# Kernel tuning notes

Measured on AMD Instinct MI355X. Metric: run time of the kernel, lower is better.

The kernel has to match this reference:

```python
import jax, jax.numpy as jnp
import numpy as np


def setup_inputs() -> dict:
    key = jax.random.key(0)
    ks = jax.random.split(key, 6)
    B, C, W, H = 8, 512, 64, 64
    return {
        "x": jax.random.normal(ks[0], (B, C, W, H), dtype=jnp.float32),
        "proj_query": jax.random.normal(ks[1], (C, W, H), dtype=jnp.float32),
        "key_w": jax.random.normal(ks[2], (C, C), dtype=jnp.float32) * 0.02,
        "key_b": jax.random.normal(ks[3], (C,), dtype=jnp.float32) * 0.02,
        "value_w": jax.random.normal(ks[4], (C, C), dtype=jnp.float32) * 0.02,
        "value_b": jax.random.normal(ks[5], (C,), dtype=jnp.float32) * 0.02,
        "gamma": jnp.ones((1,), dtype=jnp.float32),
    }


def reference(x, proj_query, key_w, key_b, value_w, value_b, gamma):
    B, C, W, H = x.shape
    N = W * H
    # fixed memory query: (C, N); torch builds B x N x C via permute
    q = proj_query.reshape(C, N)
    # 1x1 convs == per-pixel channel matmuls
    k = jnp.einsum('oc,bchw->bohw', key_w, x) + key_b[None, :, None, None]
    v = jnp.einsum('oc,bchw->bohw', value_w, x) + value_b[None, :, None, None]
    k = k.reshape(B, C, N)
    v = v.reshape(B, C, N)
    # energy = bmm(key [B,C,N], query^T [N,C]) -> B x C x C (channel attention)
    energy = jnp.einsum('bcn,dn->bcd', k, q)
    attention = jax.nn.softmax(energy, axis=-1)
    # out = bmm(attention^T [B,C,C], value [B,C,N]) -> B x C x N
    out = jnp.einsum('bdc,bdn->bcn', attention, v)
    out = out.reshape(B, C, W, H)
    return gamma * out + x
```

## Files before the change

### kernel.cpp

```cpp
#include <hip/hip_runtime.h>

typedef unsigned short u16;
typedef unsigned int u32;
typedef unsigned long long u64;
typedef _Float16 f16x8 __attribute__((ext_vector_type(8)));
typedef float f32x4 __attribute__((ext_vector_type(4)));

__device__ __forceinline__ u16 f2h(float f) {
  union { _Float16 h; u16 u; } c; c.h = (_Float16)f; return c.u;
}
__device__ __forceinline__ float h2f(u16 v) {
  union { u16 u; _Float16 h; } c; c.u = v; return (float)c.h;
}

__device__ __forceinline__ f32x4 mfma16(f16x8 a, f16x8 b, f32x4 c) {
  return __builtin_amdgcn_mfma_f32_16x16x32_f16(a, b, c, 0, 0, 0);
}

__device__ __forceinline__ void ld8f(const float* s, u16* o) {
  float4 a = *(const float4*)s;
  float4 b = *(const float4*)(s + 4);
  o[0] = f2h(a.x); o[1] = f2h(a.y); o[2] = f2h(a.z); o[3] = f2h(a.w);
  o[4] = f2h(b.x); o[5] = f2h(b.y); o[6] = f2h(b.z); o[7] = f2h(b.w);
}

__device__ __forceinline__ void cvt8(float4 a, float4 b, u16* o) {
  o[0] = f2h(a.x); o[1] = f2h(a.y); o[2] = f2h(a.z); o[3] = f2h(a.w);
  o[4] = f2h(b.x); o[5] = f2h(b.y); o[6] = f2h(b.z); o[7] = f2h(b.w);
}

__device__ __forceinline__ void glds16(const u16* g, u16* l) {
  __builtin_amdgcn_global_load_lds(
      reinterpret_cast<const __attribute__((address_space(1))) u32*>(reinterpret_cast<u64>(g)),
      reinterpret_cast<__attribute__((address_space(3))) u32*>(reinterpret_cast<u64>(l)),
      16, 0, 0);
}

template<int TM, int TN, int WM, int WN, int DEPTH>
__device__ __forceinline__ void gemm_core(const u16* __restrict__ A, int lda,
                                          const u16* __restrict__ B, int ldb,
                                          int ksteps, u16* sA, u16* sB, f32x4 acc[TM][TN]) {
  constexpr int NT = WM * WN * 64;
  constexpr int BM = WM * TM * 16, BN = WN * TN * 16;
  constexpr int TILEA = BM * 32, TILEB = BN * 32;
  constexpr int APF = (BM * 4) / NT, BPF = (BN * 4) / NT;
  constexpr int VPI = APF + BPF;
  constexpr int PF = DEPTH - 2;
  static_assert(PF == 1 || PF == 2, "");
  static_assert(APF >= 1 && BPF >= 1, "");

  const int t = threadIdx.x;
  const int lane = t & 63, wave = t >> 6;
  const int wm = wave / WN, wn = wave % WN;
  const int m16 = lane & 15, q4 = lane >> 4;

  int aoff[APF], asl[APF];
#pragma unroll
  for (int p = 0; p < APF; ++p) {
    int s = p * NT + t, row = s >> 2;
    int kc = (s & 3) ^ ((row >> 1) & 3);
    aoff[p] = row * lda + kc * 8;
    asl[p] = (p * NT + (wave << 6)) * 8;
  }
  int boff[BPF], bsl[BPF];
#pragma unroll
  for (int p = 0; p < BPF; ++p) {
    int s = p * NT + t, row = s >> 2;
    int kc = (s & 3) ^ ((row >> 1) & 3);
    boff[p] = row * ldb + kc * 8;
    bsl[p] = (p * NT + (wave << 6)) * 8;
  }

  int aro[TM], bro[TN];
#pragma unroll
  for (int i = 0; i < TM; ++i) {
    int row = wm * TM * 16 + i * 16 + m16;
    aro[i] = row * 32 + ((q4 ^ ((row >> 1) & 3)) << 3);
  }
#pragma unroll
  for (int j = 0; j < TN; ++j) {
    int row = wn * TN * 16 + j * 16 + m16;
    bro[j] = row * 32 + ((q4 ^ ((row >> 1) & 3)) << 3);
  }

#pragma unroll
  for (int j = 0; j < PF; ++j) {
    const u16* Aj = A + j * 32;
    u16* aS = sA + j * TILEA;
#pragma unroll
    for (int p = 0; p < APF; ++p) glds16(Aj + aoff[p], aS + asl[p]);
    const u16* Bj = B + j * 32;
    u16* bS = sB + j * TILEB;
#pragma unroll
    for (int p = 0; p < BPF; ++p) glds16(Bj + boff[p], bS + bsl[p]);
  }

  int cur = 0, stg = PF;
#pragma unroll 1
  for (int kt = 0; kt < ksteps; ++kt) {
    if (kt + PF < ksteps) {
      const u16* An = A + (size_t)(kt + PF) * 32;
      u16* aS = sA + stg * TILEA;
#pragma unroll
      for (int p = 0; p < APF; ++p) glds16(An + aoff[p], aS + asl[p]);
      const u16* Bn = B + (size_t)(kt + PF) * 32;
      u16* bS = sB + stg * TILEB;
#pragma unroll
      for (int p = 0; p < BPF; ++p) glds16(Bn + boff[p], bS + bsl[p]);
    }
    if (PF == 2 && kt + 2 < ksteps)
      asm volatile("s_waitcnt vmcnt(%0)" :: "n"(2 * VPI) : "memory");
    else if (kt + 1 < ksteps)
      asm volatile("s_waitcnt vmcnt(%0)" :: "n"(VPI) : "memory");
    else
      asm volatile("s_waitcnt vmcnt(0)" ::: "memory");
    __builtin_amdgcn_s_barrier();
    __builtin_amdgcn_sched_barrier(0);

    const u16* aR = sA + cur * TILEA;
    const u16* bR = sB + cur * TILEB;
    f16x8 af[TM], bv[TN];
#pragma unroll
    for (int i = 0; i < TM; ++i) af[i] = *(const f16x8*)&aR[aro[i]];
#pragma unroll
    for (int j = 0; j < TN; ++j) bv[j] = *(const f16x8*)&bR[bro[j]];
#pragma unroll
    for (int i = 0; i < TM; ++i)
#pragma unroll
      for (int j = 0; j < TN; ++j)
        acc[i][j] = mfma16(af[i], bv[j], acc[i][j]);

    cur = (cur + 1 == DEPTH) ? 0 : cur + 1;
    stg = (stg + 1 == DEPTH) ? 0 : stg + 1;
  }
}

__global__ __launch_bounds__(256) void prep_all_kernel(const float* __restrict__ x,
                                                       u16* __restrict__ xh, u16* __restrict__ xhT,
                                                       const float* __restrict__ q, u16* __restrict__ qh,
                                                       float* __restrict__ qs,
                                                       const float* __restrict__ vw, u16* __restrict__ vwT,
                                                       const float* __restrict__ kw, u16* __restrict__ kwh,
                                                       float* __restrict__ beta) {
  __shared__ __align__(16) u16 T[2 * 64 * 72];
  int blk = blockIdx.x, t = threadIdx.x;
  if (blk < 512) {
    int nt = blk & 63, b = blk >> 6;
    int s = t & 31;
    int c = (t >> 5) * 8;
    const float* xbase = x + ((size_t)b * 512 + 2 * s) * 4096 + nt * 64 + c;
    int rr = t >> 2, og = t & 3;

    float4 ca0 = *(const float4*)xbase;
    float4 ca1 = *(const float4*)(xbase + 4);
    float4 cb0 = *(const float4*)(xbase + 4096);
    float4 cb1 = *(const float4*)(xbase + 4100);

#pragma unroll 1
    for (int ot = 0; ot < 8; ++ot) {
      float4 na0, na1, nb0, nb1;
      if (ot < 7) {
        const float* np = xbase + (size_t)(ot + 1) * 64 * 4096;
        na0 = *(const float4*)np;
        na1 = *(const float4*)(np + 4);
        nb0 = *(const float4*)(np + 4096);
        nb1 = *(const float4*)(np + 4100);
      }
      u16 r0[8], r1[8];
      cvt8(ca0, ca1, r0);
      cvt8(cb0, cb1, r1);

      u16* xq = xh + ((size_t)b * 512 + ot * 64 + 2 * s) * 4096 + nt * 64 + c;
      *(int4*)xq = *(int4*)r0;
      *(int4*)(xq + 4096) = *(int4*)r1;

      u32* Tw = (u32*)(T + (ot & 1) * 4608);
#pragma unroll
      for (int e = 0; e < 8; ++e)
        Tw[(c + e) * 36 + s] = (u32)r0[e] | ((u32)r1[e] << 16);
      __syncthreads();

      const u16* Tr = T + (ot & 1) * 4608;
      int4 v0 = *(const int4*)&Tr[rr * 72 + og * 16];
      int4 v1 = *(const int4*)&Tr[rr * 72 + og * 16 + 8];
      u16* xo = xhT + ((size_t)b * 4096 + nt * 64 + rr) * 512 + ot * 64 + og * 16;
      *(int4*)xo = v0;
      *(int4*)(xo + 8) = v1;

      ca0 = na0; ca1 = na1; cb0 = nb0; cb1 = nb1;
    }
  } else if (blk < 1024) {
    int row = blk - 512;
    float s = 0.f;
#pragma unroll
    for (int p = 0; p < 2; ++p) {
      size_t i = (size_t)row * 4096 + p * 2048 + t * 8;
      u16 o[8];
      ld8f(q + i, o);
#pragma unroll
      for (int e = 0; e < 8; ++e) s += h2f(o[e]);
      *(int4*)&qh[i] = *(int4*)o;
    }
    for (int off = 32; off; off >>= 1) s += __shfl_xor(s, off);
    __shared__ float wsum[4];
    if ((t & 63) == 0) wsum[t >> 6] = s;
    __syncthreads();
    if (t == 0) qs[row] = wsum[0] + wsum[1] + wsum[2] + wsum[3];
  } else if (blk < 1280) {
    int bi = blk - 1024;
    u16* sT = T;
    int bx = bi & 15, by = bi >> 4;
#pragma unroll
    for (int p = 0; p < 4; ++p) {
      int idx = p * 256 + t; int r = idx >> 5, c = idx & 31;
      sT[r * 33 + c] = f2h(vw[(size_t)(by * 32 + r) * 512 + bx * 32 + c]);
    }
    __syncthreads();
#pragma unroll
    for (int p = 0; p < 4; ++p) {
      int idx = p * 256 + t; int r = idx >> 5, c = idx & 31;
      vwT[(size_t)(bx * 32 + r) * 512 + by * 32 + c] = sT[c * 33 + r];
    }
  } else if (blk < 1408) {
    size_t i = ((size_t)(blk - 1280) * 256 + t) * 8;
    u16 o[8];
    ld8f(kw + i, o);
    *(int4*)&kwh[i] = *(int4*)o;
  } else {
    for (int i = t; i < 4096; i += 256) beta[i] = 0.f;
  }
}

__global__ __launch_bounds__(256) void sgemm_kernel(const u16* __restrict__ qh, const u16* __restrict__ xh,
                                                    float* __restrict__ Sp0, float* __restrict__ Sp1) {
  __shared__ __align__(16) u16 sA[4 * 128 * 32], sB[4 * 128 * 32];
  int rt = blockIdx.x, jt = blockIdx.y, ks = blockIdx.z;
  int b = rt >> 2, o0 = (rt & 3) * 128;
  f32x4 acc[4][4];
#pragma unroll
  for (int i = 0; i < 4; ++i)
#pragma unroll
    for (int j = 0; j < 4; ++j) acc[i][j] = (f32x4){0.f, 0.f, 0.f, 0.f};
  gemm_core<4, 4, 2, 2, 4>(qh + (size_t)jt * 128 * 4096 + (size_t)ks * 2048, 4096,
                           xh + ((size_t)b * 512 + o0) * 4096 + (size_t)ks * 2048, 4096,
                           64, sA, sB, acc);

  const int t = threadIdx.x, lane = t & 63, wave = t >> 6;
  const int wm = wave >> 1, wn = wave & 1, m16 = lane & 15, q4 = lane >> 4;
  float* Sp = ks ? Sp1 : Sp0;
  float* Ob = Sp + (size_t)b * 262144;
#pragma unroll
  for (int i = 0; i < 4; ++i)
#pragma unroll
    for (int j = 0; j < 4; ++j)
#pragma unroll
      for (int r = 0; r < 4; ++r) {
        int y = jt * 128 + wm * 64 + i * 16 + q4 * 4 + r;
        int o = o0 + wn * 64 + j * 16 + m16;
        Ob[(size_t)y * 512 + o] = acc[i][j][r];
      }
}

__global__ __launch_bounds__(256) void sreduce_kernel(const float* __restrict__ Sp0,
                                                      const float* __restrict__ Sp1,
                                                      u16* __restrict__ Sh) {
  size_t i = ((size_t)blockIdx.x * 256 + threadIdx.x) * 8;
  float4 a0 = *(const float4*)(Sp0 + i);
  float4 a1 = *(const float4*)(Sp0 + i + 4);
  float4 b0 = *(const float4*)(Sp1 + i);
  float4 b1 = *(const float4*)(Sp1 + i + 4);
  a0.x += b0.x; a0.y += b0.y; a0.z += b0.z; a0.w += b0.w;
  a1.x += b1.x; a1.y += b1.y; a1.z += b1.z; a1.w += b1.w;
  u16 o[8];
  cvt8(a0, a1, o);
  *(int4*)&Sh[i] = *(int4*)o;
}

__global__ __launch_bounds__(256) void egemm_kernel(const u16* __restrict__ kwh, const u16* __restrict__ Sh,
                                                    float* __restrict__ E) {
  __shared__ __align__(16) u16 sA[4 * 64 * 32], sB[4 * 64 * 32];
  int xt = blockIdx.x >> 3, yt = blockIdx.x & 7, b = blockIdx.y;
  f32x4 acc[2][2];
#pragma unroll
  for (int i = 0; i < 2; ++i)
#pragma unroll
    for (int j = 0; j < 2; ++j) acc[i][j] = (f32x4){0.f, 0.f, 0.f, 0.f};
  gemm_core<2, 2, 2, 2, 4>(kwh + (size_t)xt * 64 * 512, 512,
                           Sh + (size_t)b * 262144 + (size_t)yt * 64 * 512, 512, 16, sA, sB, acc);

  const int t = threadIdx.x, lane = t & 63, wave = t >> 6;
  const int wm = wave >> 1, wn = wave & 1, m16 = lane & 15, q4 = lane >> 4;
  float* O = E + ((size_t)b * 512 + xt * 64) * 512 + yt * 64;
#pragma unroll
  for (int i = 0; i < 2; ++i)
#pragma unroll
    for (int j = 0; j < 2; ++j)
#pragma unroll
      for (int r = 0; r < 4; ++r) {
        int row = wm * 32 + i * 16 + q4 * 4 + r;
        int col = wn * 32 + j * 16 + m16;
        O[(size_t)row * 512 + col] = acc[i][j][r];
      }
}

__global__ __launch_bounds__(256) void softmax_kernel(const float* __restrict__ E, const float* __restrict__ qs,
                                                      const float* __restrict__ kb, const float* __restrict__ vb,
                                                      u16* __restrict__ attT, float* __restrict__ beta) {
  __shared__ float sE[16 * 516];
  __shared__ float sM[16], sS[16];
  int i0 = blockIdx.x * 16, b = blockIdx.y, t = threadIdx.x;
  const float* Eb = E + ((size_t)b * 512 + i0) * 512;
  for (int ch = 0; ch < 32; ++ch) {
    int idx = ch * 256 + t;
    int row = idx >> 9, col = idx & 511;
    sE[row * 516 + col] = Eb[(size_t)row * 512 + col] + kb[i0 + row] * qs[col];
  }
  __syncthreads();
  {
    int row = t >> 4, sub = t & 15;
    float mx = -1e30f;
    for (int ii = 0; ii < 32; ++ii) mx = fmaxf(mx, sE[row * 516 + sub + ii * 16]);
    for (int off = 8; off; off >>= 1) mx = fmaxf(mx, __shfl_xor(mx, off));
    float sm = 0.f;
    for (int ii = 0; ii < 32; ++ii) sm += __expf(sE[row * 516 + sub + ii * 16] - mx);
    for (int off = 8; off; off >>= 1) sm += __shfl_xor(sm, off);
    if (sub == 0) { sM[row] = mx; sS[row] = 1.f / sm; }
  }
  __syncthreads();
  float vbr = vb[i0 + (t & 15)];
  u16* Ob = attT + (size_t)b * 262144;
  for (int ch = 0; ch < 32; ++ch) {
    int idx = ch * 256 + t;
    int r = idx & 15, j = idx >> 4;
    float a = __expf(sE[r * 516 + j] - sM[r]) * sS[r];
    Ob[(size_t)j * 512 + i0 + r] = f2h(a);
    float part = a * vbr;
    for (int off = 8; off; off >>= 1) part += __shfl_xor(part, off);
    if (r == 0) atomicAdd(&beta[b * 512 + j], part);
  }
}

__global__ __launch_bounds__(256) void wgemm_kernel(const u16* __restrict__ attT, const u16* __restrict__ vwT,
                                                    u16* __restrict__ W) {
  __shared__ __align__(16) u16 sA[4 * 64 * 32], sB[4 * 64 * 32];
  int ct = blockIdx.x >> 3, ot = blockIdx.x & 7, b = blockIdx.y;
  f32x4 acc[2][2];
#pragma unroll
  for (int i = 0; i < 2; ++i)
#pragma unroll
    for (int j = 0; j < 2; ++j) acc[i][j] = (f32x4){0.f, 0.f, 0.f, 0.f};
  gemm_core<2, 2, 2, 2, 4>(attT + (size_t)b * 262144 + (size_t)ct * 64 * 512, 512,
                           vwT + (size_t)ot * 64 * 512, 512, 16, sA, sB, acc);

  const int t = threadIdx.x, lane = t & 63, wave = t >> 6;
  const int wm = wave >> 1, wn = wave & 1, m16 = lane & 15, q4 = lane >> 4;
  u16* O = W + (size_t)b * 262144 + (size_t)(ct * 64) * 512 + ot * 64;
#pragma unroll
  for (int i = 0; i < 2; ++i)
#pragma unroll
    for (int j = 0; j < 2; ++j)
#pragma unroll
      for (int r = 0; r < 4; ++r) {
        int row = wm * 32 + i * 16 + q4 * 4 + r;
        int col = wn * 32 + j * 16 + m16;
        O[(size_t)row * 512 + col] = f2h(acc[i][j][r]);
      }
}

__global__ __launch_bounds__(256) void outgemm_kernel(const u16* __restrict__ W, const u16* __restrict__ xhT,
                                                      const float* __restrict__ x, const float* __restrict__ beta,
                                                      const float* __restrict__ gm, float* __restrict__ out) {
  __shared__ __align__(16) u16 sA[4 * 128 * 32], sB[4 * 128 * 32];
  int nt = blockIdx.x, ct = blockIdx.y, b = blockIdx.z;
  f32x4 acc[4][4];
#pragma unroll
  for (int i = 0; i < 4; ++i)
#pragma unroll
    for (int j = 0; j < 4; ++j) acc[i][j] = (f32x4){0.f, 0.f, 0.f, 0.f};
  gemm_core<4, 4, 2, 2, 4>(W + (size_t)b * 262144 + (size_t)ct * 128 * 512, 512,
                           xhT + (size_t)b * 2097152 + (size_t)nt * 128 * 512, 512, 16, sA, sB, acc);

  const int t = threadIdx.x, lane = t & 63, wave = t >> 6;
  const int wm = wave >> 1, wn = wave & 1, m16 = lane & 15, q4 = lane >> 4;
  float g = gm[0];
#pragma unroll
  for (int i = 0; i < 4; ++i)
#pragma unroll
    for (int j = 0; j < 4; ++j)
#pragma unroll
      for (int r = 0; r < 4; ++r) {
        int c = ct * 128 + wm * 64 + i * 16 + q4 * 4 + r;
        int n = nt * 128 + wn * 64 + j * 16 + m16;
        size_t idx = (size_t)b * 2097152 + (size_t)c * 4096 + n;
        out[idx] = g * (acc[i][j][r] + beta[b * 512 + c]) + x[idx];
      }
}

extern "C" void kernel_launch(void* const* d_in, const int* in_sizes, int n_in,
                              void* d_out, int out_size, void* d_ws, size_t ws_size,
                              hipStream_t stream) {
  const float* x  = (const float*)d_in[0];
  const float* pq = (const float*)d_in[1];
  const float* kw = (const float*)d_in[2];
  const float* kb = (const float*)d_in[3];
  const float* vw = (const float*)d_in[4];
  const float* vb = (const float*)d_in[5];
  const float* gm = (const float*)d_in[6];
  float* out = (float*)d_out;

  char* ws = (char*)d_ws;
  u16*   xh   = (u16*)(ws);
  u16*   qh   = (u16*)(ws + (32ull << 20));
  u16*   Sh   = (u16*)(ws + (36ull << 20));
  u16*   W    = (u16*)(ws + (36ull << 20));
  float* E    = (float*)(ws + (40ull << 20));
  float* Sp0  = (float*)(ws + (40ull << 20));
  u16*   attT = (u16*)(ws + (48ull << 20));
  u16*   kwh  = (u16*)(ws + (52ull << 20));
  u16*   vwT  = (u16*)(ws + (52ull << 20) + 524288);
  char*  sm   = ws + (53ull << 20);
  float* qs   = (float*)(sm);
  float* beta = (float*)(sm + 4096);
  u16*   xhT  = (u16*)(ws + (54ull << 20));
  float* Sp1  = (float*)(ws + (86ull << 20));

  prep_all_kernel<<<dim3(1409), 256, 0, stream>>>(x, xh, xhT, pq, qh, qs, vw, vwT, kw, kwh, beta);
  sgemm_kernel<<<dim3(32, 4, 2), 256, 0, stream>>>(qh, xh, Sp0, Sp1);
  sreduce_kernel<<<dim3(1024), 256, 0, stream>>>(Sp0, Sp1, Sh);
  egemm_kernel<<<dim3(64, 8), 256, 0, stream>>>(kwh, Sh, E);
  softmax_kernel<<<dim3(32, 8), 256, 0, stream>>>(E, qs, kb, vb, attT, beta);
  wgemm_kernel<<<dim3(64, 8), 256, 0, stream>>>(attT, vwT, W);
  outgemm_kernel<<<dim3(32, 4, 8), 256, 0, stream>>>(W, xhT, x, beta, gm, out);
}
```

Before: 238.5 us.

## Swizzle block indices batch-innermost for XCD locality and retile x transpose prep

Every kernel now uses a 1D grid with the batch index in the low bits of blockIdx. Consecutive blocks therefore spread across batches, which on MI355X's round-robin XCD dispatch keeps each batch's blocks on the same XCD and its L2. The x-prep stage also changes from 512 blocks that each loop over 8 channel tiles with double-buffered LDS to 1024 blocks. Each new block converts a 128x128 tile with a single sync and writes 128-byte transposed rows. The cost is more LDS per block and register pressure from the 32-wide register array in the transpose.

Result: slower. 249.2 us (+4.5%).

```diff
diff --git a/kernel.cpp b/kernel.cpp
--- a/kernel.cpp
+++ b/kernel.cpp
@@ -142,55 +142,44 @@
                                                        const float* __restrict__ vw, u16* __restrict__ vwT,
                                                        const float* __restrict__ kw, u16* __restrict__ kwh,
                                                        float* __restrict__ beta) {
-  __shared__ __align__(16) u16 T[2 * 64 * 72];
+  __shared__ __align__(16) u32 T[128 * 65];
   int blk = blockIdx.x, t = threadIdx.x;
-  if (blk < 512) {
-    int nt = blk & 63, b = blk >> 6;
-    int s = t & 31;
-    int c = (t >> 5) * 8;
-    const float* xbase = x + ((size_t)b * 512 + 2 * s) * 4096 + nt * 64 + c;
-    int rr = t >> 2, og = t & 3;
-
-    float4 ca0 = *(const float4*)xbase;
-    float4 ca1 = *(const float4*)(xbase + 4);
-    float4 cb0 = *(const float4*)(xbase + 4096);
-    float4 cb1 = *(const float4*)(xbase + 4100);
-
-#pragma unroll 1
-    for (int ot = 0; ot < 8; ++ot) {
-      float4 na0, na1, nb0, nb1;
-      if (ot < 7) {
-        const float* np = xbase + (size_t)(ot + 1) * 64 * 4096;
-        na0 = *(const float4*)np;
-        na1 = *(const float4*)(np + 4);
-        nb0 = *(const float4*)(np + 4096);
-        nb1 = *(const float4*)(np + 4100);
-      }
-      u16 r0[8], r1[8];
-      cvt8(ca0, ca1, r0);
-      cvt8(cb0, cb1, r1);
-
-      u16* xq = xh + ((size_t)b * 512 + ot * 64 + 2 * s) * 4096 + nt * 64 + c;
-      *(int4*)xq = *(int4*)r0;
-      *(int4*)(xq + 4096) = *(int4*)r1;
-
-      u32* Tw = (u32*)(T + (ot & 1) * 4608);
+  if (blk < 1024) {
+    int b = blk & 7, r = blk >> 3;
+    int nt = r & 31, ot = r >> 5;
+    int rp = t & 63, qw = t >> 6;
+    int o0 = ot * 128 + 2 * rp;
+    int n0 = nt * 128 + qw * 32;
+    const float* x0 = x + ((size_t)b * 512 + o0) * 4096 + n0;
+    u16* xq = xh + ((size_t)b * 512 + o0) * 4096 + n0;
+
+#pragma unroll
+    for (int k = 0; k < 4; ++k) {
+      float4 a0 = *(const float4*)(x0 + 8 * k);
+      float4 a1 = *(const float4*)(x0 + 8 * k + 4);
+      float4 b0 = *(const float4*)(x0 + 4096 + 8 * k);
+      float4 b1 = *(const float4*)(x0 + 4096 + 8 * k + 4);
+      u16 h0[8], h1[8];
+      cvt8(a0, a1, h0);
+      cvt8(b0, b1, h1);
+      *(int4*)(xq + 8 * k) = *(int4*)h0;
+      *(int4*)(xq + 4096 + 8 * k) = *(int4*)h1;
 #pragma unroll
       for (int e = 0; e < 8; ++e)
-        Tw[(c + e) * 36 + s] = (u32)r0[e] | ((u32)r1[e] << 16);
-      __syncthreads();
-
-      const u16* Tr = T + (ot & 1) * 4608;
-      int4 v0 = *(const int4*)&Tr[rr * 72 + og * 16];
-      int4 v1 = *(const int4*)&Tr[rr * 72 + og * 16 + 8];
-      u16* xo = xhT + ((size_t)b * 4096 + nt * 64 + rr) * 512 + ot * 64 + og * 16;
-      *(int4*)xo = v0;
-      *(int4*)(xo + 8) = v1;
-
-      ca0 = na0; ca1 = na1; cb0 = nb0; cb1 = nb1;
+        T[(qw * 32 + 8 * k + e) * 65 + rp] = (u32)h0[e] | ((u32)h1[e] << 16);
     }
-  } else if (blk < 1024) {
-    int row = blk - 512;
+    __syncthreads();
+
+    int n = t >> 1, hh = t & 1;
+    u32 v[32];
+#pragma unroll
+    for (int j = 0; j < 32; ++j) v[j] = T[n * 65 + hh * 32 + j];
+    u16* xo = xhT + ((size_t)b * 4096 + nt * 128 + n) * 512 + ot * 128 + hh * 64;
+#pragma unroll
+    for (int j = 0; j < 8; ++j)
+      *(int4*)(xo + 8 * j) = *(int4*)&v[4 * j];
+  } else if (blk < 1536) {
+    int row = blk - 1024;
     float s = 0.f;
 #pragma unroll
     for (int p = 0; p < 2; ++p) {
@@ -206,9 +195,9 @@
     if ((t & 63) == 0) wsum[t >> 6] = s;
     __syncthreads();
     if (t == 0) qs[row] = wsum[0] + wsum[1] + wsum[2] + wsum[3];
-  } else if (blk < 1280) {
-    int bi = blk - 1024;
-    u16* sT = T;
+  } else if (blk < 1792) {
+    int bi = blk - 1536;
+    u16* sT = (u16*)T;
     int bx = bi & 15, by = bi >> 4;
 #pragma unroll
     for (int p = 0; p < 4; ++p) {
@@ -221,8 +210,8 @@
       int idx = p * 256 + t; int r = idx >> 5, c = idx & 31;
       vwT[(size_t)(bx * 32 + r) * 512 + by * 32 + c] = sT[c * 33 + r];
     }
-  } else if (blk < 1408) {
-    size_t i = ((size_t)(blk - 1280) * 256 + t) * 8;
+  } else if (blk < 1920) {
+    size_t i = ((size_t)(blk - 1792) * 256 + t) * 8;
     u16 o[8];
     ld8f(kw + i, o);
     *(int4*)&kwh[i] = *(int4*)o;
@@ -234,8 +223,10 @@
 __global__ __launch_bounds__(256) void sgemm_kernel(const u16* __restrict__ qh, const u16* __restrict__ xh,
                                                     float* __restrict__ Sp0, float* __restrict__ Sp1) {
   __shared__ __align__(16) u16 sA[4 * 128 * 32], sB[4 * 128 * 32];
-  int rt = blockIdx.x, jt = blockIdx.y, ks = blockIdx.z;
-  int b = rt >> 2, o0 = (rt & 3) * 128;
+  int blk = blockIdx.x;
+  int b = blk & 7, r = blk >> 3;
+  int och = r & 3, jt = (r >> 2) & 3, ks = r >> 4;
+  int o0 = och * 128;
   f32x4 acc[4][4];
 #pragma unroll
   for (int i = 0; i < 4; ++i)
@@ -254,17 +245,19 @@
 #pragma unroll
     for (int j = 0; j < 4; ++j)
 #pragma unroll
-      for (int r = 0; r < 4; ++r) {
-        int y = jt * 128 + wm * 64 + i * 16 + q4 * 4 + r;
+      for (int r2 = 0; r2 < 4; ++r2) {
+        int y = jt * 128 + wm * 64 + i * 16 + q4 * 4 + r2;
         int o = o0 + wn * 64 + j * 16 + m16;
-        Ob[(size_t)y * 512 + o] = acc[i][j][r];
+        Ob[(size_t)y * 512 + o] = acc[i][j][r2];
       }
 }
 
 __global__ __launch_bounds__(256) void sreduce_kernel(const float* __restrict__ Sp0,
                                                       const float* __restrict__ Sp1,
                                                       u16* __restrict__ Sh) {
-  size_t i = ((size_t)blockIdx.x * 256 + threadIdx.x) * 8;
+  int blk = blockIdx.x;
+  int b = blk & 7, r = blk >> 3;
+  size_t i = (size_t)b * 262144 + (size_t)r * 2048 + threadIdx.x * 8;
   float4 a0 = *(const float4*)(Sp0 + i);
   float4 a1 = *(const float4*)(Sp0 + i + 4);
   float4 b0 = *(const float4*)(Sp1 + i);
@@ -279,7 +272,9 @@
 __global__ __launch_bounds__(256) void egemm_kernel(const u16* __restrict__ kwh, const u16* __restrict__ Sh,
                                                     float* __restrict__ E) {
   __shared__ __align__(16) u16 sA[4 * 64 * 32], sB[4 * 64 * 32];
-  int xt = blockIdx.x >> 3, yt = blockIdx.x & 7, b = blockIdx.y;
+  int blk = blockIdx.x;
+  int b = blk & 7, r = blk >> 3;
+  int xt = r >> 3, yt = r & 7;
   f32x4 acc[2][2];
 #pragma unroll
   for (int i = 0; i < 2; ++i)
@@ -296,10 +291,10 @@
 #pragma unroll
     for (int j = 0; j < 2; ++j)
 #pragma unroll
-      for (int r = 0; r < 4; ++r) {
-        int row = wm * 32 + i * 16 + q4 * 4 + r;
+      for (int r2 = 0; r2 < 4; ++r2) {
+        int row = wm * 32 + i * 16 + q4 * 4 + r2;
         int col = wn * 32 + j * 16 + m16;
-        O[(size_t)row * 512 + col] = acc[i][j][r];
+        O[(size_t)row * 512 + col] = acc[i][j][r2];
       }
 }
 
@@ -308,7 +303,9 @@
                                                       u16* __restrict__ attT, float* __restrict__ beta) {
   __shared__ float sE[16 * 516];
   __shared__ float sM[16], sS[16];
-  int i0 = blockIdx.x * 16, b = blockIdx.y, t = threadIdx.x;
+  int blk = blockIdx.x;
+  int b = blk & 7, i0 = (blk >> 3) * 16;
+  int t = threadIdx.x;
   const float* Eb = E + ((size_t)b * 512 + i0) * 512;
   for (int ch = 0; ch < 32; ++ch) {
     int idx = ch * 256 + t;
@@ -343,7 +340,9 @@
 __global__ __launch_bounds__(256) void wgemm_kernel(const u16* __restrict__ attT, const u16* __restrict__ vwT,
                                                     u16* __restrict__ W) {
   __shared__ __align__(16) u16 sA[4 * 64 * 32], sB[4 * 64 * 32];
-  int ct = blockIdx.x >> 3, ot = blockIdx.x & 7, b = blockIdx.y;
+  int blk = blockIdx.x;
+  int b = blk & 7, r = blk >> 3;
+  int ct = r >> 3, ot = r & 7;
   f32x4 acc[2][2];
 #pragma unroll
   for (int i = 0; i < 2; ++i)
@@ -360,10 +359,10 @@
 #pragma unroll
     for (int j = 0; j < 2; ++j)
 #pragma unroll
-      for (int r = 0; r < 4; ++r) {
-        int row = wm * 32 + i * 16 + q4 * 4 + r;
+      for (int r2 = 0; r2 < 4; ++r2) {
+        int row = wm * 32 + i * 16 + q4 * 4 + r2;
         int col = wn * 32 + j * 16 + m16;
-        O[(size_t)row * 512 + col] = f2h(acc[i][j][r]);
+        O[(size_t)row * 512 + col] = f2h(acc[i][j][r2]);
       }
 }
 
@@ -371,7 +370,9 @@
                                                       const float* __restrict__ x, const float* __restrict__ beta,
                                                       const float* __restrict__ gm, float* __restrict__ out) {
   __shared__ __align__(16) u16 sA[4 * 128 * 32], sB[4 * 128 * 32];
-  int nt = blockIdx.x, ct = blockIdx.y, b = blockIdx.z;
+  int blk = blockIdx.x;
+  int b = blk & 7, r = blk >> 3;
+  int nt = r & 31, ct = r >> 5;
   f32x4 acc[4][4];
 #pragma unroll
   for (int i = 0; i < 4; ++i)
@@ -388,11 +389,11 @@
 #pragma unroll
     for (int j = 0; j < 4; ++j)
 #pragma unroll
-      for (int r = 0; r < 4; ++r) {
-        int c = ct * 128 + wm * 64 + i * 16 + q4 * 4 + r;
+      for (int r2 = 0; r2 < 4; ++r2) {
+        int c = ct * 128 + wm * 64 + i * 16 + q4 * 4 + r2;
         int n = nt * 128 + wn * 64 + j * 16 + m16;
         size_t idx = (size_t)b * 2097152 + (size_t)c * 4096 + n;
-        out[idx] = g * (acc[i][j][r] + beta[b * 512 + c]) + x[idx];
+        out[idx] = g * (acc[i][j][r2] + beta[b * 512 + c]) + x[idx];
       }
 }
 
@@ -424,11 +425,11 @@
   u16*   xhT  = (u16*)(ws + (54ull << 20));
   float* Sp1  = (float*)(ws + (86ull << 20));
 
-  prep_all_kernel<<<dim3(1409), 256, 0, stream>>>(x, xh, xhT, pq, qh, qs, vw, vwT, kw, kwh, beta);
-  sgemm_kernel<<<dim3(32, 4, 2), 256, 0, stream>>>(qh, xh, Sp0, Sp1);
+  prep_all_kernel<<<dim3(1921), 256, 0, stream>>>(x, xh, xhT, pq, qh, qs, vw, vwT, kw, kwh, beta);
+  sgemm_kernel<<<dim3(256), 256, 0, stream>>>(qh, xh, Sp0, Sp1);
   sreduce_kernel<<<dim3(1024), 256, 0, stream>>>(Sp0, Sp1, Sh);
-  egemm_kernel<<<dim3(64, 8), 256, 0, stream>>>(kwh, Sh, E);
-  softmax_kernel<<<dim3(32, 8), 256, 0, stream>>>(E, qs, kb, vb, attT, beta);
-  wgemm_kernel<<<dim3(64, 8), 256, 0, stream>>>(attT, vwT, W);
-  outgemm_kernel<<<dim3(32, 4, 8), 256, 0, stream>>>(W, xhT, x, beta, gm, out);
-}
+  egemm_kernel<<<dim3(512), 256, 0, stream>>>(kwh, Sh, E);
+  softmax_kernel<<<dim3(256), 256, 0, stream>>>(E, qs, kb, vb, attT, beta);
+  wgemm_kernel<<<dim3(512), 256, 0, stream>>>(attT, vwT, W);
+  outgemm_kernel<<<dim3(1024), 256, 0, stream>>>(W, xhT, x, beta, gm, out);
+}
```

## Fuse split-K partial reduction and fp16 conversion into energy GEMM B-operand load

Applied to the files above, without the earlier changes.

Removes the separate sreduce kernel. The energy GEMM now loads both fp32 split-K partials of S directly, adds them, converts to fp16, and writes them into a triple-buffered LDS B tile with register prefetch two steps ahead. The whole 64x512 kw tile is preloaded into LDS with async global-to-LDS loads. This saves one launch and the round trip of the fp16 S buffer. In exchange, each egemm block (64 x 8 grid) reads 2x fp32 data redundantly across the 8 xt tiles, and E is moved to a new workspace offset.

New measurement: 242.3 us. About the same (+1.6%).

```diff
diff --git a/kernel.cpp b/kernel.cpp
--- a/kernel.cpp
+++ b/kernel.cpp
@@ -27,6 +27,11 @@
 __device__ __forceinline__ void cvt8(float4 a, float4 b, u16* o) {
   o[0] = f2h(a.x); o[1] = f2h(a.y); o[2] = f2h(a.z); o[3] = f2h(a.w);
   o[4] = f2h(b.x); o[5] = f2h(b.y); o[6] = f2h(b.z); o[7] = f2h(b.w);
+}
+
+__device__ __forceinline__ void addcvt8(float4 a0, float4 a1, float4 c0, float4 c1, u16* o) {
+  o[0] = f2h(a0.x + c0.x); o[1] = f2h(a0.y + c0.y); o[2] = f2h(a0.z + c0.z); o[3] = f2h(a0.w + c0.w);
+  o[4] = f2h(a1.x + c1.x); o[5] = f2h(a1.y + c1.y); o[6] = f2h(a1.z + c1.z); o[7] = f2h(a1.w + c1.w);
 }
 
 __device__ __forceinline__ void glds16(const u16* g, u16* l) {
@@ -254,52 +259,116 @@
 #pragma unroll
     for (int j = 0; j < 4; ++j)
 #pragma unroll
-      for (int r = 0; r < 4; ++r) {
-        int y = jt * 128 + wm * 64 + i * 16 + q4 * 4 + r;
+      for (int r2 = 0; r2 < 4; ++r2) {
+        int y = jt * 128 + wm * 64 + i * 16 + q4 * 4 + r2;
         int o = o0 + wn * 64 + j * 16 + m16;
-        Ob[(size_t)y * 512 + o] = acc[i][j][r];
+        Ob[(size_t)y * 512 + o] = acc[i][j][r2];
       }
 }
 
-__global__ __launch_bounds__(256) void sreduce_kernel(const float* __restrict__ Sp0,
-                                                      const float* __restrict__ Sp1,
-                                                      u16* __restrict__ Sh) {
-  size_t i = ((size_t)blockIdx.x * 256 + threadIdx.x) * 8;
-  float4 a0 = *(const float4*)(Sp0 + i);
-  float4 a1 = *(const float4*)(Sp0 + i + 4);
-  float4 b0 = *(const float4*)(Sp1 + i);
-  float4 b1 = *(const float4*)(Sp1 + i + 4);
-  a0.x += b0.x; a0.y += b0.y; a0.z += b0.z; a0.w += b0.w;
-  a1.x += b1.x; a1.y += b1.y; a1.z += b1.z; a1.w += b1.w;
-  u16 o[8];
-  cvt8(a0, a1, o);
-  *(int4*)&Sh[i] = *(int4*)o;
-}
-
-__global__ __launch_bounds__(256) void egemm_kernel(const u16* __restrict__ kwh, const u16* __restrict__ Sh,
+__global__ __launch_bounds__(256) void egemm_kernel(const u16* __restrict__ kwh,
+                                                    const float* __restrict__ Sp0,
+                                                    const float* __restrict__ Sp1,
                                                     float* __restrict__ E) {
-  __shared__ __align__(16) u16 sA[4 * 64 * 32], sB[4 * 64 * 32];
+  __shared__ __align__(16) u16 sA[16 * 2048];
+  __shared__ __align__(16) u16 sB[3 * 2048];
   int xt = blockIdx.x >> 3, yt = blockIdx.x & 7, b = blockIdx.y;
-  f32x4 acc[2][2];
-#pragma unroll
-  for (int i = 0; i < 2; ++i)
-#pragma unroll
-    for (int j = 0; j < 2; ++j) acc[i][j] = (f32x4){0.f, 0.f, 0.f, 0.f};
-  gemm_core<2, 2, 2, 2, 4>(kwh + (size_t)xt * 64 * 512, 512,
-                           Sh + (size_t)b * 262144 + (size_t)yt * 64 * 512, 512, 16, sA, sB, acc);
-
   const int t = threadIdx.x, lane = t & 63, wave = t >> 6;
   const int wm = wave >> 1, wn = wave & 1, m16 = lane & 15, q4 = lane >> 4;
+
+  {
+    int row = t >> 2;
+    int kc = (t & 3) ^ ((row >> 1) & 3);
+    const u16* Abase = kwh + (size_t)(xt * 64 + row) * 512 + kc * 8;
+    u16* adst = sA + (t & 192) * 8;
+#pragma unroll
+    for (int k2 = 0; k2 < 16; ++k2)
+      glds16(Abase + k2 * 32, adst + k2 * 2048);
+  }
+
+  int srow = t >> 2;
+  int skc = (t & 3) ^ ((srow >> 1) & 3);
+  const float* b0 = Sp0 + (size_t)b * 262144 + (size_t)(yt * 64 + srow) * 512 + skc * 8;
+  const float* b1 = Sp1 + (size_t)b * 262144 + (size_t)(yt * 64 + srow) * 512 + skc * 8;
+
+  float4 pa0, pa1, pa2, pa3, pb0, pb1, pb2, pb3;
+  pa0 = *(const float4*)(b0);      pa1 = *(const float4*)(b0 + 4);
+  pa2 = *(const float4*)(b1);      pa3 = *(const float4*)(b1 + 4);
+  pb0 = *(const float4*)(b0 + 32); pb1 = *(const float4*)(b0 + 36);
+  pb2 = *(const float4*)(b1 + 32); pb3 = *(const float4*)(b1 + 36);
+  {
+    u16 h[8];
+    addcvt8(pa0, pa1, pa2, pa3, h);
+    *(int4*)&sB[t * 8] = *(int4*)h;
+  }
+  asm volatile("s_waitcnt vmcnt(0) lgkmcnt(0)" ::: "memory");
+  __builtin_amdgcn_s_barrier();
+
+  int aro[2], bro[2];
+#pragma unroll
+  for (int i = 0; i < 2; ++i) {
+    int row = wm * 32 + i * 16 + m16;
+    aro[i] = row * 32 + ((q4 ^ ((row >> 1) & 3)) << 3);
+  }
+#pragma unroll
+  for (int j = 0; j < 2; ++j) {
+    int row = wn * 32 + j * 16 + m16;
+    bro[j] = row * 32 + ((q4 ^ ((row >> 1) & 3)) << 3);
+  }
+
+  f32x4 acc[2][2];
+#pragma unroll
+  for (int i = 0; i < 2; ++i)
+#pragma unroll
+    for (int j = 0; j < 2; ++j) acc[i][j] = (f32x4){0.f, 0.f, 0.f, 0.f};
+
+#pragma unroll 2
+  for (int kt = 0; kt < 16; ++kt) {
+    if (kt + 2 < 16) {
+      const float* s0 = b0 + (kt + 2) * 32;
+      const float* s1 = b1 + (kt + 2) * 32;
+      if (kt & 1) {
+        pb0 = *(const float4*)s0; pb1 = *(const float4*)(s0 + 4);
+        pb2 = *(const float4*)s1; pb3 = *(const float4*)(s1 + 4);
+      } else {
+        pa0 = *(const float4*)s0; pa1 = *(const float4*)(s0 + 4);
+        pa2 = *(const float4*)s1; pa3 = *(const float4*)(s1 + 4);
+      }
+    }
+    if (kt + 1 < 16) {
+      u16 h[8];
+      if (kt & 1) addcvt8(pa0, pa1, pa2, pa3, h);
+      else        addcvt8(pb0, pb1, pb2, pb3, h);
+      *(int4*)&sB[((kt + 1) % 3) * 2048 + t * 8] = *(int4*)h;
+    }
+    asm volatile("s_waitcnt lgkmcnt(0)" ::: "memory");
+    __builtin_amdgcn_s_barrier();
+    __builtin_amdgcn_sched_barrier(0);
+
+    const u16* aT = sA + kt * 2048;
+    const u16* bT = sB + (kt % 3) * 2048;
+    f16x8 af[2], bv[2];
+#pragma unroll
+    for (int i = 0; i < 2; ++i) af[i] = *(const f16x8*)&aT[aro[i]];
+#pragma unroll
+    for (int j = 0; j < 2; ++j) bv[j] = *(const f16x8*)&bT[bro[j]];
+#pragma unroll
+    for (int i = 0; i < 2; ++i)
+#pragma unroll
+      for (int j = 0; j < 2; ++j)
+        acc[i][j] = mfma16(af[i], bv[j], acc[i][j]);
+  }
+
   float* O = E + ((size_t)b * 512 + xt * 64) * 512 + yt * 64;
 #pragma unroll
   for (int i = 0; i < 2; ++i)
 #pragma unroll
     for (int j = 0; j < 2; ++j)
 #pragma unroll
-      for (int r = 0; r < 4; ++r) {
-        int row = wm * 32 + i * 16 + q4 * 4 + r;
+      for (int r2 = 0; r2 < 4; ++r2) {
+        int row = wm * 32 + i * 16 + q4 * 4 + r2;
         int col = wn * 32 + j * 16 + m16;
-        O[(size_t)row * 512 + col] = acc[i][j][r];
+        O[(size_t)row * 512 + col] = acc[i][j][r2];
       }
 }
 
@@ -360,10 +429,10 @@
 #pragma unroll
     for (int j = 0; j < 2; ++j)
 #pragma unroll
-      for (int r = 0; r < 4; ++r) {
-        int row = wm * 32 + i * 16 + q4 * 4 + r;
+      for (int r2 = 0; r2 < 4; ++r2) {
+        int row = wm * 32 + i * 16 + q4 * 4 + r2;
         int col = wn * 32 + j * 16 + m16;
-        O[(size_t)row * 512 + col] = f2h(acc[i][j][r]);
+        O[(size_t)row * 512 + col] = f2h(acc[i][j][r2]);
       }
 }
 
@@ -388,11 +457,11 @@
 #pragma unroll
     for (int j = 0; j < 4; ++j)
 #pragma unroll
-      for (int r = 0; r < 4; ++r) {
-        int c = ct * 128 + wm * 64 + i * 16 + q4 * 4 + r;
+      for (int r2 = 0; r2 < 4; ++r2) {
+        int c = ct * 128 + wm * 64 + i * 16 + q4 * 4 + r2;
         int n = nt * 128 + wn * 64 + j * 16 + m16;
         size_t idx = (size_t)b * 2097152 + (size_t)c * 4096 + n;
-        out[idx] = g * (acc[i][j][r] + beta[b * 512 + c]) + x[idx];
+        out[idx] = g * (acc[i][j][r2] + beta[b * 512 + c]) + x[idx];
       }
 }
 
@@ -411,9 +480,8 @@
   char* ws = (char*)d_ws;
   u16*   xh   = (u16*)(ws);
   u16*   qh   = (u16*)(ws + (32ull << 20));
-  u16*   Sh   = (u16*)(ws + (36ull << 20));
+  float* E    = (float*)(ws + (32ull << 20));
   u16*   W    = (u16*)(ws + (36ull << 20));
-  float* E    = (float*)(ws + (40ull << 20));
   float* Sp0  = (float*)(ws + (40ull << 20));
   u16*   attT = (u16*)(ws + (48ull << 20));
   u16*   kwh  = (u16*)(ws + (52ull << 20));
@@ -426,8 +494,7 @@
 
   prep_all_kernel<<<dim3(1409), 256, 0, stream>>>(x, xh, xhT, pq, qh, qs, vw, vwT, kw, kwh, beta);
   sgemm_kernel<<<dim3(32, 4, 2), 256, 0, stream>>>(qh, xh, Sp0, Sp1);
-  sreduce_kernel<<<dim3(1024), 256, 0, stream>>>(Sp0, Sp1, Sh);
-  egemm_kernel<<<dim3(64, 8), 256, 0, stream>>>(kwh, Sh, E);
+  egemm_kernel<<<dim3(64, 8), 256, 0, stream>>>(kwh, Sp0, Sp1, E);
   softmax_kernel<<<dim3(32, 8), 256, 0, stream>>>(E, qs, kb, vb, attT, beta);
   wgemm_kernel<<<dim3(64, 8), 256, 0, stream>>>(attT, vwT, W);
   outgemm_kernel<<<dim3(32, 4, 8), 256, 0, stream>>>(W, xhT, x, beta, gm, out);
```
